# Performance work log

Hardware: AMD Instinct MI355X
Metric: run time of the kernel (lower is better)

Reference implementation:

```python
import jax, jax.numpy as jnp
import numpy as np

T, B, OBS, H, A = 128, 256, 128, 512, 18
LSTM_IN = H + A + 1  # trunk_out + one_hot(a) + r


def setup_inputs() -> dict:
    key = jax.random.key(0)
    ks = jax.random.split(key, 24)

    def rn(k, shape, scale=0.05):
        return jax.random.normal(k, shape, dtype=jnp.float32) * scale

    inp = {
        "o": jax.random.normal(ks[0], (T, B, OBS), dtype=jnp.float32),
        "a": jax.random.randint(ks[1], (T, B), 0, A, dtype=jnp.int32),
        "r": jax.random.normal(ks[2], (T, B), dtype=jnp.float32),
        "done": (jax.random.uniform(ks[3], (T, B)) < 0.05).astype(jnp.float32),
        "h0": jax.random.normal(ks[4], (B, H), dtype=jnp.float32) * 0.1,
        "c0": jax.random.normal(ks[5], (B, H), dtype=jnp.float32) * 0.1,
        # trunk
        "tW0": rn(ks[6], (OBS, H)), "tb0": jnp.zeros((H,), jnp.float32),
        "tW1": rn(ks[7], (H, H)), "tb1": jnp.zeros((H,), jnp.float32),
        # LSTM (PyTorch layout: gates stacked as [i, f, g, o])
        "W_ih": rn(ks[8], (4 * H, LSTM_IN)), "W_hh": rn(ks[9], (4 * H, H)),
        "b_ih": jnp.zeros((4 * H,), jnp.float32), "b_hh": jnp.zeros((4 * H,), jnp.float32),
        # advantage head
        "aW0": rn(ks[10], (H, H)), "ab0": jnp.zeros((H,), jnp.float32),
        "aW1": rn(ks[11], (H, A)), "ab1": jnp.zeros((A,), jnp.float32),
        # value head
        "vW0": rn(ks[12], (H, H)), "vb0": jnp.zeros((H,), jnp.float32),
        "vW1": rn(ks[13], (H, 1)), "vb1": jnp.zeros((1,), jnp.float32),
    }
    return inp


def _forward(o, a, r, done, h0, c0, tW0, tb0, tW1, tb1,
             W_ih, W_hh, b_ih, b_hh, aW0, ab0, aW1, ab1, vW0, vb0, vW1, vb1):
    # shared trunk: two Linear+ReLU layers, vectorized over T*B
    hidden = jax.nn.relu(jnp.einsum('tbi,ih->tbh', o, tW0) + tb0)
    hidden = jax.nn.relu(jnp.einsum('tbi,ih->tbh', hidden, tW1) + tb1)
    a_oh = jax.nn.one_hot(a, A, dtype=jnp.float32)          # [T,B,A]
    x = jnp.concatenate([hidden, r[..., None], a_oh], -1)    # [T,B,LSTM_IN]

    # precompute input projection for all steps (not state-dependent)
    xg = jnp.einsum('tbi,gi->tbg', x, W_ih) + b_ih + b_hh    # [T,B,4H]

    def step(carry, inp):
        h, c = carry
        xg_t, d_t = inp
        keep = (1.0 - d_t)[:, None]                          # per-step done reset
        h, c = h * keep, c * keep
        gates = xg_t + h @ W_hh.T                            # [B,4H]
        i, f, g, og = jnp.split(gates, 4, axis=-1)
        c = jax.nn.sigmoid(f) * c + jax.nn.sigmoid(i) * jnp.tanh(g)
        h = jax.nn.sigmoid(og) * jnp.tanh(c)
        return (h, c), h

    (hT, cT), hs = jax.lax.scan(step, (h0, c0), (xg, done))  # hs: [T,B,H]

    ah = jax.nn.relu(jnp.einsum('tbh,hk->tbk', hs, aW0) + ab0)
    adv = jnp.einsum('tbk,ka->tba', ah, aW1) + ab1            # [T,B,A]
    vh = jax.nn.relu(jnp.einsum('tbh,hk->tbk', hs, vW0) + vb0)
    val = jnp.einsum('tbk,kv->tbv', vh, vW1) + vb1            # [T,B,1]
    q = val + (adv - adv.mean(axis=-1, keepdims=True))
    return q, hT, cT


def reference(o, a, r, done, h0, c0, tW0, tb0, tW1, tb1,
              W_ih, W_hh, b_ih, b_hh, aW0, ab0, aW1, ab1, vW0, vb0, vW1, vb1):
    return _forward(o, a, r, done, h0, c0, tW0, tb0, tW1, tb1,
                    W_ih, W_hh, b_ih, b_hh, aW0, ab0, aW1, ab1, vW0, vb0, vW1, vb1)
```

## Files before the change

### kernel.cpp

```cpp
#include <hip/hip_runtime.h>
#include <cstdint>

typedef unsigned short u16;
typedef unsigned int u32;
typedef unsigned long long u64;
typedef float f32x4 __attribute__((ext_vector_type(4)));
typedef short s16x8 __attribute__((ext_vector_type(8)));

#define DEV static __device__ __forceinline__

#define TT 128
#define BB 256
#define OBSD 128
#define HHD 512
#define AD 18
#define GGD 2048
#define MMD 32768

DEV u16 f2bf(float f) {
  u32 u = __builtin_bit_cast(u32, f);
  u += 0x7fffu + ((u >> 16) & 1u);
  return (u16)(u >> 16);
}
DEV float bf2f(u16 h) { return __builtin_bit_cast(float, ((u32)h) << 16); }

DEV f32x4 mfma16x16x32(s16x8 a, s16x8 b, f32x4 c) {
  asm("v_mfma_f32_16x16x32_bf16 %0, %1, %2, %0" : "+v"(c) : "v"(a), "v"(b));
  return c;
}
DEV void fence_mfma_read(f32x4& x) { asm volatile("s_nop 7" : "+v"(x)); }
DEV void fence_mfma_srcc(f32x4& x) { asm volatile("s_nop 1" : "+v"(x)); }
DEV void fence_valu_srca(s16x8& x) { asm volatile("s_nop 1" : "+v"(x)); }

typedef __attribute__((address_space(3))) char lds_char;
typedef __attribute__((address_space(1))) const char gl_char;
DEV void gload16(const char* g, char* l) {
  __builtin_amdgcn_global_load_lds((const gl_char*)g, (lds_char*)l, 16, 0, 0);
}

DEV float sigm(float x) { return 1.f / (1.f + __expf(-x)); }
DEV float tanh_fast(float x) {
  float t = __expf(-2.f * fabsf(x));
  float r = (1.f - t) / (1.f + t);
  return copysignf(r, x);
}

constexpr size_t OFF_FLAGS = 0;
constexpr size_t OFF_HRING = 524288;
constexpr size_t OFF_TW0T  = 1048576;
constexpr size_t OFF_TW1T  = 1179648;
constexpr size_t OFF_AW0T  = 1703936;
constexpr size_t OFF_VW0T  = 2228224;
constexpr size_t OFF_AW1T  = 2752512;
constexpr size_t OFF_VW1T  = 2770944;
constexpr size_t OFF_WIH   = 2772992;
constexpr size_t OFF_WHH   = 4870144;
constexpr size_t OFF_BSUM  = 6967296;
constexpr size_t OFF_WRC   = 6975488;
constexpr size_t OFF_WEMB  = 6983680;
constexpr size_t OFF_BCAT  = 7131136;
constexpr size_t OFF_OBF   = 8388608;
constexpr size_t OFF_BUF1  = 16777216;
constexpr size_t OFF_BUF2  = 50331648;
constexpr size_t OFF_BUF3  = 83886080;

__global__ __launch_bounds__(256) void prep(
    const float* __restrict__ o, const float* __restrict__ tW0,
    const float* __restrict__ tW1, const float* __restrict__ aW0,
    const float* __restrict__ vW0, const float* __restrict__ aW1,
    const float* __restrict__ vW1, const float* __restrict__ Wih,
    const float* __restrict__ WhhF, const float* __restrict__ bih,
    const float* __restrict__ bhh, const float* __restrict__ h0,
    const float* __restrict__ ab0, const float* __restrict__ vb0,
    u16* __restrict__ o_bf, u16* __restrict__ tW0T, u16* __restrict__ tW1T,
    u16* __restrict__ aW0T, u16* __restrict__ vW0T, u16* __restrict__ aW1T,
    u16* __restrict__ vW1T, u16* __restrict__ WihB, u16* __restrict__ WhhB,
    float* __restrict__ bsum, float* __restrict__ wrc, float* __restrict__ wemb,
    float* __restrict__ bcat, u16* __restrict__ hring)
{
  const int total = 4178432;
  for (int id = blockIdx.x * 256 + threadIdx.x; id < total; id += gridDim.x * 256) {
    int i = id;
    if (i < 1048576) {
      float4 v = ((const float4*)o)[i];
      u16* dst = o_bf + (size_t)i * 4;
      dst[0] = f2bf(v.x); dst[1] = f2bf(v.y); dst[2] = f2bf(v.z); dst[3] = f2bf(v.w);
      continue;
    }
    i -= 1048576;
    if (i < 65536)  { int n = i >> 7, k = i & 127; tW0T[i] = f2bf(tW0[k * 512 + n]); continue; }
    i -= 65536;
    if (i < 262144) { int n = i >> 9, k = i & 511; tW1T[i] = f2bf(tW1[k * 512 + n]); continue; }
    i -= 262144;
    if (i < 262144) { int n = i >> 9, k = i & 511; aW0T[i] = f2bf(aW0[k * 512 + n]); continue; }
    i -= 262144;
    if (i < 262144) { int n = i >> 9, k = i & 511; vW0T[i] = f2bf(vW0[k * 512 + n]); continue; }
    i -= 262144;
    if (i < 9216)   { int n = i >> 9, k = i & 511; aW1T[i] = f2bf(aW1[k * 18 + n]); continue; }
    i -= 9216;
    if (i < 512)    { vW1T[i] = f2bf(vW1[i]); continue; }
    i -= 512;
    if (i < 1048576){ int g = i >> 9, k = i & 511; WihB[i] = f2bf(Wih[g * 531 + k]); continue; }
    i -= 1048576;
    if (i < 1048576){ WhhB[i] = f2bf(WhhF[i]); continue; }
    i -= 1048576;
    if (i < 2048)   { bsum[i] = bih[i] + bhh[i]; wrc[i] = Wih[i * 531 + 512]; continue; }
    i -= 2048;
    if (i < 36864)  { int j = i >> 11, g = i & 2047; wemb[i] = Wih[g * 531 + 513 + j]; continue; }
    i -= 36864;
    if (i < 1024)   { bcat[i] = (i < 512) ? ab0[i] : vb0[i - 512]; continue; }
    i -= 1024;
    { hring[i] = f2bf(h0[i]); }
  }
}

template<int MODE>
__global__ __launch_bounds__(256) void gemm_bt(
    const u16* __restrict__ A, const u16* __restrict__ Bt, u16* __restrict__ C,
    int Mdim, int Ndim, int Kdim,
    const float* __restrict__ bias,
    const float* __restrict__ wrc, const float* __restrict__ wemb,
    const float* __restrict__ rin, const int* __restrict__ ain)
{
  __shared__ __align__(16) char smem[32768];
  const int tid = threadIdx.x;
  const int nTn = Ndim >> 7;
  int wg = blockIdx.x;
  {
    const int per = gridDim.x >> 3;
    wg = (wg & 7) * per + (wg >> 3);
  }
  const int tm = wg / nTn, tn = wg % nTn;
  const int wid = tid >> 6, lane = tid & 63;
  const int wr = wid >> 1, wc = wid & 1;
  const int l15 = lane & 15, l4 = lane >> 4;

  f32x4 acc[4][4];
#pragma unroll
  for (int i = 0; i < 4; ++i)
#pragma unroll
    for (int j = 0; j < 4; ++j) acc[i][j] = f32x4{0.f, 0.f, 0.f, 0.f};

  const int srow = lane >> 3;
  const int scolb = ((lane & 7) * 16) ^ (srow << 4);
  const size_t kd2 = (size_t)Kdim * 2;
  const char* Abase = (const char*)(A + (size_t)tm * 128 * Kdim);
  const char* Bbase = (const char*)(Bt + (size_t)tn * 128 * Kdim);
  const char* ga[4]; const char* gb[4]; char* la[4]; char* lb[4];
#pragma unroll
  for (int j = 0; j < 4; ++j) {
    const int row = wid * 32 + j * 8 + srow;
    ga[j] = Abase + (size_t)row * kd2 + scolb;
    gb[j] = Bbase + (size_t)row * kd2 + scolb;
    la[j] = smem + wid * 4096 + j * 1024;
    lb[j] = smem + 16384 + wid * 4096 + j * 1024;
  }

  for (int k0 = 0; k0 < Kdim; k0 += 64) {
    const size_t kb = (size_t)k0 * 2;
#pragma unroll
    for (int j = 0; j < 4; ++j) {
      gload16(ga[j] + kb, la[j]);
      gload16(gb[j] + kb, lb[j]);
    }
    __syncthreads();
#pragma unroll
    for (int kk = 0; kk < 2; ++kk) {
      s16x8 af[4], bfr[4];
#pragma unroll
      for (int i = 0; i < 4; ++i) {
        int ar = wr * 64 + i * 16 + l15;
        af[i] = *(const s16x8*)(smem + ((ar * 128 + kk * 64 + l4 * 16) ^ ((ar & 7) << 4)));
        int br = wc * 64 + i * 16 + l15;
        bfr[i] = *(const s16x8*)(smem + 16384 + ((br * 128 + kk * 64 + l4 * 16) ^ ((br & 7) << 4)));
      }
#pragma unroll
      for (int i = 0; i < 4; ++i)
#pragma unroll
        for (int j = 0; j < 4; ++j)
          acc[i][j] = mfma16x16x32(af[i], bfr[j], acc[i][j]);
    }
    __syncthreads();
  }

#pragma unroll
  for (int i = 0; i < 4; ++i)
#pragma unroll
    for (int j = 0; j < 4; ++j) fence_mfma_read(acc[i][j]);

#pragma unroll
  for (int i = 0; i < 4; ++i) {
    const int rowb = tm * 128 + wr * 64 + i * 16 + l4 * 4;
    float rv[4]; int av[4];
    if (MODE == 1) {
#pragma unroll
      for (int r = 0; r < 4; ++r) { rv[r] = rin[rowb + r]; av[r] = ain[rowb + r]; }
    }
#pragma unroll
    for (int j = 0; j < 4; ++j) {
      const int col = tn * 128 + wc * 64 + j * 16 + l15;
      const float bs = bias[col];
      if (MODE == 0) {
#pragma unroll
        for (int r = 0; r < 4; ++r) {
          float x = acc[i][j][r] + bs;
          x = fmaxf(x, 0.f);
          C[(size_t)(rowb + r) * Ndim + col] = f2bf(x);
        }
      } else {
        const float wcv = wrc[col];
#pragma unroll
        for (int r = 0; r < 4; ++r) {
          float x = acc[i][j][r] + bs + rv[r] * wcv + wemb[av[r] * GGD + col];
          C[(size_t)(rowb + r) * Ndim + col] = f2bf(x);
        }
      }
    }
  }
}

__global__ __launch_bounds__(256, 1) void lstm_seq(
    const u16* __restrict__ xg, const u16* __restrict__ WhhB,
    const u16* __restrict__ WheadT, const float* __restrict__ done,
    const float* __restrict__ c0, const float* __restrict__ bcat,
    u16* __restrict__ hring, u16* __restrict__ ah, u16* __restrict__ vh,
    float* __restrict__ hT, float* __restrict__ cT, u32* __restrict__ cnt)
{
  __shared__ __align__(16) char wsm[65536];
  __shared__ __align__(16) char whd[32768];
  const int tid = threadIdx.x;
  const int bg = blockIdx.x & 3;
  const int ug = blockIdx.x >> 2;
  const int b0 = bg * 64;
  const int u0 = ug * 16;
  const int hc0 = ug * 32;

#pragma unroll
  for (int i = 0; i < 16; ++i) {
    int idx = i * 256 + tid;
    int lr = idx >> 6, c8 = idx & 63;
    int g = lr >> 4, uu = lr & 15;
    uint4 v = *(const uint4*)(WhhB + (size_t)(g * 512 + u0 + uu) * 512 + c8 * 8);
    *(uint4*)(wsm + ((lr * 1024 + c8 * 16) ^ ((lr & 7) << 4))) = v;
  }
#pragma unroll
  for (int i = 0; i < 8; ++i) {
    int idx = i * 256 + tid;
    int lr = idx >> 6, c8 = idx & 63;
    uint4 v = *(const uint4*)(WheadT + (size_t)(hc0 + lr) * 512 + c8 * 8);
    *(uint4*)(whd + ((lr * 1024 + c8 * 16) ^ ((lr & 7) << 4))) = v;
  }
  __syncthreads();

  const int wid = tid >> 6, lane = tid & 63;
  const int l15 = lane & 15, l4 = lane >> 4;
  const int mrow = wid * 16 + l4 * 4;
  const int afrow = b0 + wid * 16 + l15;
  const int u = u0 + l15;
  u32* const mycnt = cnt + ((bg << 2) | wid) * TT;

  u16* const hvout = (ug < 16) ? ah : vh;
  const int hcl = (ug < 16) ? hc0 : hc0 - 512;
  float bcv[2];
#pragma unroll
  for (int j = 0; j < 2; ++j) bcv[j] = bcat[hc0 + j * 16 + l15];

  float creg[4], kc[4];
#pragma unroll
  for (int r = 0; r < 4; ++r) {
    creg[r] = c0[(size_t)(b0 + mrow + r) * HHD + u];
    kc[r] = 1.f - done[b0 + mrow + r];
  }
  u64 am;
  { float dn = done[afrow]; am = (dn != 0.f) ? 0ull : ~0ull; }

  u16 xpf[16];
#pragma unroll
  for (int g = 0; g < 4; ++g)
#pragma unroll
    for (int r = 0; r < 4; ++r)
      xpf[g * 4 + r] = xg[(size_t)(b0 + mrow + r) * GGD + g * HHD + u];

  for (int t = 0; t < TT; ++t) {
    const u16* hsrc = hring + (size_t)(t & 1) * (BB * HHD);
    u16* hdst = hring + (size_t)((t + 1) & 1) * (BB * HHD);

    f32x4 acc[4];
#pragma unroll
    for (int g = 0; g < 4; ++g)
#pragma unroll
      for (int r = 0; r < 4; ++r)
        acc[g][r] = bf2f(xpf[g * 4 + r]);
#pragma unroll
    for (int g = 0; g < 4; ++g) fence_mfma_srcc(acc[g]);

    u64 aflo[16], afhi[16];
    const u64* hb = (const u64*)(hsrc + (size_t)afrow * HHD);
#pragma unroll
    for (int kk = 0; kk < 16; ++kk) {
      aflo[kk] = __hip_atomic_load(hb + kk * 8 + l4 * 2,
                                   __ATOMIC_RELAXED, __HIP_MEMORY_SCOPE_AGENT);
      afhi[kk] = __hip_atomic_load(hb + kk * 8 + l4 * 2 + 1,
                                   __ATOMIC_RELAXED, __HIP_MEMORY_SCOPE_AGENT);
    }
#pragma unroll
    for (int kk = 0; kk < 16; ++kk) {
      union { u64 q[2]; s16x8 v; } tmp;
      tmp.q[0] = aflo[kk] & am; tmp.q[1] = afhi[kk] & am;
      s16x8 a = tmp.v;
      fence_valu_srca(a);
#pragma unroll
      for (int g = 0; g < 4; ++g) {
        int br = g * 16 + l15;
        s16x8 b = *(const s16x8*)(wsm + ((br * 1024 + kk * 64 + l4 * 16) ^ ((br & 7) << 4)));
        acc[g] = mfma16x16x32(a, b, acc[g]);
      }
    }
#pragma unroll
    for (int g = 0; g < 4; ++g) fence_mfma_read(acc[g]);

    float hv_[4], cv_[4];
#pragma unroll
    for (int r = 0; r < 4; ++r) {
      float iv = sigm(acc[0][r]);
      float fv = sigm(acc[1][r]);
      float gv = tanh_fast(acc[2][r]);
      float ov = sigm(acc[3][r]);
      float c = fv * (creg[r] * kc[r]) + iv * gv;
      float h = ov * tanh_fast(c);
      creg[r] = c; cv_[r] = c; hv_[r] = h;
    }

    {
      u32 pw[4];
#pragma unroll
      for (int r = 0; r < 4; ++r) {
        u16 ob = f2bf(hv_[r]);
        u16 pb = (u16)__shfl_xor((int)ob, 1, 64);
        pw[r] = ((l15 & 1) == 0) ? ((u32)ob | ((u32)pb << 16))
                                 : ((u32)pb | ((u32)ob << 16));
      }
      const int rb = (l15 & 1) * 2;
      u32* hd32 = (u32*)hdst;
      const int col2 = (u0 + (l15 & ~1)) >> 1;
      __hip_atomic_store(&hd32[(size_t)(b0 + mrow + rb) * 256 + col2], pw[rb],
                         __ATOMIC_RELAXED, __HIP_MEMORY_SCOPE_AGENT);
      __hip_atomic_store(&hd32[(size_t)(b0 + mrow + rb + 1) * 256 + col2], pw[rb + 1],
                         __ATOMIC_RELAXED, __HIP_MEMORY_SCOPE_AGENT);
    }
    asm volatile("s_waitcnt vmcnt(0)" ::: "memory");
    if (lane == 0)
      __hip_atomic_fetch_add(&mycnt[t], 1u,
                             __ATOMIC_RELAXED, __HIP_MEMORY_SCOPE_AGENT);

    if (t > 0) {
      f32x4 acch[2];
#pragma unroll
      for (int j = 0; j < 2; ++j)
#pragma unroll
        for (int r = 0; r < 4; ++r) acch[j][r] = bcv[j];
#pragma unroll
      for (int j = 0; j < 2; ++j) fence_mfma_srcc(acch[j]);
#pragma unroll
      for (int kk = 0; kk < 16; ++kk) {
        union { u64 q[2]; s16x8 v; } tmp;
        tmp.q[0] = aflo[kk]; tmp.q[1] = afhi[kk];
        s16x8 a = tmp.v;
#pragma unroll
        for (int j = 0; j < 2; ++j) {
          int br = j * 16 + l15;
          s16x8 b = *(const s16x8*)(whd + ((br * 1024 + kk * 64 + l4 * 16) ^ ((br & 7) << 4)));
          acch[j] = mfma16x16x32(a, b, acch[j]);
        }
      }
#pragma unroll
      for (int j = 0; j < 2; ++j) fence_mfma_read(acch[j]);
#pragma unroll
      for (int j = 0; j < 2; ++j)
#pragma unroll
        for (int r = 0; r < 4; ++r) {
          float x = fmaxf(acch[j][r], 0.f);
          hvout[((size_t)(t - 1) * BB + b0 + mrow + r) * 512 + hcl + j * 16 + l15] = f2bf(x);
        }
    }
    if (t == TT - 1) {
#pragma unroll
      for (int r = 0; r < 4; ++r) {
        hT[(size_t)(b0 + mrow + r) * HHD + u] = hv_[r];
        cT[(size_t)(b0 + mrow + r) * HHD + u] = cv_[r];
      }
    } else {
#pragma unroll
      for (int g = 0; g < 4; ++g)
#pragma unroll
        for (int r = 0; r < 4; ++r)
          xpf[g * 4 + r] = xg[((size_t)(t + 1) * BB + b0 + mrow + r) * GGD + g * HHD + u];
#pragma unroll
      for (int r = 0; r < 4; ++r)
        kc[r] = 1.f - done[(size_t)(t + 1) * BB + b0 + mrow + r];
      float dn = done[(size_t)(t + 1) * BB + afrow];
      am = (dn != 0.f) ? 0ull : ~0ull;
    }

    while (__hip_atomic_load(&mycnt[t],
                             __ATOMIC_RELAXED, __HIP_MEMORY_SCOPE_AGENT) < 32u)
      __builtin_amdgcn_s_sleep(1);
  }

  {
    const u16* hfin = hring + (size_t)(TT & 1) * (BB * HHD);
    u64 aflo[16], afhi[16];
    const u64* hb = (const u64*)(hfin + (size_t)afrow * HHD);
#pragma unroll
    for (int kk = 0; kk < 16; ++kk) {
      aflo[kk] = __hip_atomic_load(hb + kk * 8 + l4 * 2,
                                   __ATOMIC_RELAXED, __HIP_MEMORY_SCOPE_AGENT);
      afhi[kk] = __hip_atomic_load(hb + kk * 8 + l4 * 2 + 1,
                                   __ATOMIC_RELAXED, __HIP_MEMORY_SCOPE_AGENT);
    }
    f32x4 acch[2];
#pragma unroll
    for (int j = 0; j < 2; ++j)
#pragma unroll
      for (int r = 0; r < 4; ++r) acch[j][r] = bcv[j];
#pragma unroll
    for (int j = 0; j < 2; ++j) fence_mfma_srcc(acch[j]);
#pragma unroll
    for (int kk = 0; kk < 16; ++kk) {
      union { u64 q[2]; s16x8 v; } tmp;
      tmp.q[0] = aflo[kk]; tmp.q[1] = afhi[kk];
      s16x8 a = tmp.v;
#pragma unroll
      for (int j = 0; j < 2; ++j) {
        int br = j * 16 + l15;
        s16x8 b = *(const s16x8*)(whd + ((br * 1024 + kk * 64 + l4 * 16) ^ ((br & 7) << 4)));
        acch[j] = mfma16x16x32(a, b, acch[j]);
      }
    }
#pragma unroll
    for (int j = 0; j < 2; ++j) fence_mfma_read(acch[j]);
#pragma unroll
    for (int j = 0; j < 2; ++j)
#pragma unroll
      for (int r = 0; r < 4; ++r) {
        float x = fmaxf(acch[j][r], 0.f);
        hvout[((size_t)(TT - 1) * BB + b0 + mrow + r) * 512 + hcl + j * 16 + l15] = f2bf(x);
      }
  }
}

__global__ __launch_bounds__(256) void head_final(
    const u16* __restrict__ ah, const u16* __restrict__ vh,
    const u16* __restrict__ aW1T, const u16* __restrict__ vW1T,
    const float* __restrict__ ab1, const float* __restrict__ vb1,
    float* __restrict__ q)
{
  __shared__ __align__(16) u16 wa[AD * HHD];
  __shared__ __align__(16) u16 wv[HHD];
  const int tid = threadIdx.x;
  for (int i = tid; i < AD * HHD / 8; i += 256) ((uint4*)wa)[i] = ((const uint4*)aW1T)[i];
  for (int i = tid; i < HHD / 8; i += 256) ((uint4*)wv)[i] = ((const uint4*)vW1T)[i];
  __syncthreads();
  const int wid = tid >> 6, lane = tid & 63;
  for (int row = blockIdx.x * 4 + wid; row < MMD; row += gridDim.x * 4) {
    uint4 va = *(const uint4*)(ah + (size_t)row * 512 + lane * 8);
    uint4 vv = *(const uint4*)(vh + (size_t)row * 512 + lane * 8);
    const u16* pa = (const u16*)&va;
    const u16* pv = (const u16*)&vv;
    float af[8], vf[8];
#pragma unroll
    for (int j = 0; j < 8; ++j) { af[j] = bf2f(pa[j]); vf[j] = bf2f(pv[j]); }
    float accs[19];
#pragma unroll
    for (int n = 0; n < 19; ++n) accs[n] = 0.f;
#pragma unroll
    for (int n = 0; n < AD; ++n) {
      const u16* w = wa + n * HHD + lane * 8;
#pragma unroll
      for (int j = 0; j < 8; ++j) accs[n] += af[j] * bf2f(w[j]);
    }
    {
      const u16* w = wv + lane * 8;
#pragma unroll
      for (int j = 0; j < 8; ++j) accs[18] += vf[j] * bf2f(w[j]);
    }
#pragma unroll
    for (int n = 0; n < 19; ++n) {
#pragma unroll
      for (int off = 32; off > 0; off >>= 1)
        accs[n] += __shfl_xor(accs[n], off, 64);
    }
    if (lane == 0) {
      float s = 0.f;
      float advv[AD];
#pragma unroll
      for (int n = 0; n < AD; ++n) { advv[n] = accs[n] + ab1[n]; s += advv[n]; }
      float val = accs[18] + vb1[0];
      float mean = s * (1.f / 18.f);
#pragma unroll
      for (int n = 0; n < AD; ++n) q[(size_t)row * AD + n] = val + advv[n] - mean;
    }
  }
}

extern "C" void kernel_launch(void* const* d_in, const int* in_sizes, int n_in,
                              void* d_out, int out_size, void* d_ws, size_t ws_size,
                              hipStream_t stream) {
  const float* o    = (const float*)d_in[0];
  const int*   a    = (const int*)d_in[1];
  const float* r    = (const float*)d_in[2];
  const float* done = (const float*)d_in[3];
  const float* h0   = (const float*)d_in[4];
  const float* c0   = (const float*)d_in[5];
  const float* tW0  = (const float*)d_in[6];
  const float* tb0  = (const float*)d_in[7];
  const float* tW1  = (const float*)d_in[8];
  const float* tb1  = (const float*)d_in[9];
  const float* Wih  = (const float*)d_in[10];
  const float* Whh  = (const float*)d_in[11];
  const float* bih  = (const float*)d_in[12];
  const float* bhh  = (const float*)d_in[13];
  const float* aW0  = (const float*)d_in[14];
  const float* ab0  = (const float*)d_in[15];
  const float* aW1  = (const float*)d_in[16];
  const float* ab1  = (const float*)d_in[17];
  const float* vW0  = (const float*)d_in[18];
  const float* vb0  = (const float*)d_in[19];
  const float* vW1  = (const float*)d_in[20];
  const float* vb1  = (const float*)d_in[21];
  (void)in_sizes; (void)n_in; (void)ws_size;

  char* ws = (char*)d_ws;
  u32* cnt    = (u32*)(ws + OFF_FLAGS);
  u16* hring  = (u16*)(ws + OFF_HRING);
  u16* tW0T   = (u16*)(ws + OFF_TW0T);
  u16* tW1T   = (u16*)(ws + OFF_TW1T);
  u16* aW0T   = (u16*)(ws + OFF_AW0T);
  u16* vW0T   = (u16*)(ws + OFF_VW0T);
  u16* aW1T   = (u16*)(ws + OFF_AW1T);
  u16* vW1T   = (u16*)(ws + OFF_VW1T);
  u16* WihB   = (u16*)(ws + OFF_WIH);
  u16* WhhB   = (u16*)(ws + OFF_WHH);
  float* bsum = (float*)(ws + OFF_BSUM);
  float* wrc  = (float*)(ws + OFF_WRC);
  float* wemb = (float*)(ws + OFF_WEMB);
  float* bcat = (float*)(ws + OFF_BCAT);
  u16* o_bf   = (u16*)(ws + OFF_OBF);
  u16* buf1   = (u16*)(ws + OFF_BUF1);
  u16* buf2   = (u16*)(ws + OFF_BUF2);
  u16* buf3   = (u16*)(ws + OFF_BUF3);

  float* qout = (float*)d_out;
  float* hT   = qout + (size_t)TT * BB * AD;
  float* cT   = hT + (size_t)BB * HHD;

  hipMemsetAsync(cnt, 0, 65536, stream);
  prep<<<2048, 256, 0, stream>>>(o, tW0, tW1, aW0, vW0, aW1, vW1, Wih, Whh,
                                 bih, bhh, h0, ab0, vb0,
                                 o_bf, tW0T, tW1T, aW0T, vW0T, aW1T, vW1T,
                                 WihB, WhhB, bsum, wrc, wemb, bcat, hring);
  gemm_bt<0><<<1024, 256, 0, stream>>>(o_bf, tW0T, buf1, MMD, 512, 128, tb0,
                                       nullptr, nullptr, nullptr, nullptr);
  gemm_bt<0><<<1024, 256, 0, stream>>>(buf1, tW1T, buf2, MMD, 512, 512, tb1,
                                       nullptr, nullptr, nullptr, nullptr);
  gemm_bt<1><<<4096, 256, 0, stream>>>(buf2, WihB, buf3, MMD, 2048, 512, bsum,
                                       wrc, wemb, r, a);
  lstm_seq<<<128, 256, 0, stream>>>(buf3, WhhB, aW0T, done, c0, bcat, hring,
                                    buf1 , buf2 , hT, cT, cnt);
  head_final<<<2048, 256, 0, stream>>>(buf1, buf2, aW1T, vW1T, ab1, vb1, qout);
}
```

Baseline: 1.012 ms.

## Fuse input-projection GEMM into LSTM scan kernel with per-tile ready flags

The separate xg GEMM launch is folded into one kernel with the recurrent scan. Extra blocks compute the projection tiles and store them with agent-scope atomic stores, then bump a per-tile flag. The LSTM blocks spin on those flags before prefetching each step's gate inputs. The goal is to hide the projection GEMM behind the serial recurrence instead of running it beforehand. In exchange it relies on all recurrent blocks being resident alongside the producers, adds flag-polling overhead, and lets producer blocks contend with the scan for bandwidth and CUs.

```diff
diff --git a/kernel.cpp b/kernel.cpp
--- a/kernel.cpp
+++ b/kernel.cpp
@@ -46,6 +46,7 @@
 }
 
 constexpr size_t OFF_FLAGS = 0;
+constexpr size_t OFF_XGFLG = 32768;
 constexpr size_t OFF_HRING = 524288;
 constexpr size_t OFF_TW0T  = 1048576;
 constexpr size_t OFF_TW1T  = 1179648;
@@ -114,13 +115,9 @@
   }
 }
 
-template<int MODE>
 __global__ __launch_bounds__(256) void gemm_bt(
     const u16* __restrict__ A, const u16* __restrict__ Bt, u16* __restrict__ C,
-    int Mdim, int Ndim, int Kdim,
-    const float* __restrict__ bias,
-    const float* __restrict__ wrc, const float* __restrict__ wemb,
-    const float* __restrict__ rin, const int* __restrict__ ain)
+    int Mdim, int Ndim, int Kdim, const float* __restrict__ bias)
 {
   __shared__ __align__(16) char smem[32768];
   const int tid = threadIdx.x;
@@ -191,49 +188,137 @@
 #pragma unroll
   for (int i = 0; i < 4; ++i) {
     const int rowb = tm * 128 + wr * 64 + i * 16 + l4 * 4;
-    float rv[4]; int av[4];
-    if (MODE == 1) {
-#pragma unroll
-      for (int r = 0; r < 4; ++r) { rv[r] = rin[rowb + r]; av[r] = ain[rowb + r]; }
-    }
 #pragma unroll
     for (int j = 0; j < 4; ++j) {
       const int col = tn * 128 + wc * 64 + j * 16 + l15;
       const float bs = bias[col];
-      if (MODE == 0) {
-#pragma unroll
-        for (int r = 0; r < 4; ++r) {
-          float x = acc[i][j][r] + bs;
-          x = fmaxf(x, 0.f);
-          C[(size_t)(rowb + r) * Ndim + col] = f2bf(x);
+#pragma unroll
+      for (int r = 0; r < 4; ++r) {
+        float x = acc[i][j][r] + bs;
+        x = fmaxf(x, 0.f);
+        C[(size_t)(rowb + r) * Ndim + col] = f2bf(x);
+      }
+    }
+  }
+}
+
+__global__ __launch_bounds__(256, 1) void scan_fused(
+    const u16* __restrict__ hid, const u16* __restrict__ WihB,
+    const float* __restrict__ rin, const int* __restrict__ ain,
+    const float* __restrict__ bsum, const float* __restrict__ wrcv,
+    const float* __restrict__ wemb, u16* __restrict__ xg,
+    const u16* __restrict__ WhhB, const u16* __restrict__ WheadT,
+    const float* __restrict__ done, const float* __restrict__ c0,
+    const float* __restrict__ bcat, u16* __restrict__ hring,
+    u16* __restrict__ ah, u16* __restrict__ vh,
+    float* __restrict__ hT, float* __restrict__ cT,
+    u32* __restrict__ cnt, u32* __restrict__ xgflag)
+{
+  __shared__ __align__(16) char lds[98304];
+  const int tid = threadIdx.x;
+  const int wid = tid >> 6, lane = tid & 63;
+  const int l15 = lane & 15, l4 = lane >> 4;
+
+  if (blockIdx.x >= 128) {
+    char* smem = lds;
+    const int wr = wid >> 1, wc = wid & 1;
+    const int srow = lane >> 3;
+    const int scolb = ((lane & 7) * 16) ^ (srow << 4);
+    const int wkr = blockIdx.x - 128;
+    for (int idx = wkr; idx < 4096; idx += 512) {
+      const int tm = idx >> 4, tn = idx & 15;
+      f32x4 acc[4][4];
+#pragma unroll
+      for (int i = 0; i < 4; ++i)
+#pragma unroll
+        for (int j = 0; j < 4; ++j) acc[i][j] = f32x4{0.f, 0.f, 0.f, 0.f};
+      const char* Abase = (const char*)(hid + (size_t)tm * 128 * 512);
+      const char* Bbase = (const char*)(WihB + (size_t)tn * 128 * 512);
+      const char* ga[4]; const char* gb[4]; char* la[4]; char* lb[4];
+#pragma unroll
+      for (int j = 0; j < 4; ++j) {
+        const int row = wid * 32 + j * 8 + srow;
+        ga[j] = Abase + (size_t)row * 1024 + scolb;
+        gb[j] = Bbase + (size_t)row * 1024 + scolb;
+        la[j] = smem + wid * 4096 + j * 1024;
+        lb[j] = smem + 16384 + wid * 4096 + j * 1024;
+      }
+      for (int k0 = 0; k0 < 512; k0 += 64) {
+        const size_t kb = (size_t)k0 * 2;
+#pragma unroll
+        for (int j = 0; j < 4; ++j) {
+          gload16(ga[j] + kb, la[j]);
+          gload16(gb[j] + kb, lb[j]);
         }
-      } else {
-        const float wcv = wrc[col];
-#pragma unroll
-        for (int r = 0; r < 4; ++r) {
-          float x = acc[i][j][r] + bs + rv[r] * wcv + wemb[av[r] * GGD + col];
-          C[(size_t)(rowb + r) * Ndim + col] = f2bf(x);
+        __syncthreads();
+#pragma unroll
+        for (int kk = 0; kk < 2; ++kk) {
+          s16x8 af[4], bfr[4];
+#pragma unroll
+          for (int i = 0; i < 4; ++i) {
+            int ar = wr * 64 + i * 16 + l15;
+            af[i] = *(const s16x8*)(smem + ((ar * 128 + kk * 64 + l4 * 16) ^ ((ar & 7) << 4)));
+            int br = wc * 64 + i * 16 + l15;
+            bfr[i] = *(const s16x8*)(smem + 16384 + ((br * 128 + kk * 64 + l4 * 16) ^ ((br & 7) << 4)));
+          }
+#pragma unroll
+          for (int i = 0; i < 4; ++i)
+#pragma unroll
+            for (int j = 0; j < 4; ++j)
+              acc[i][j] = mfma16x16x32(af[i], bfr[j], acc[i][j]);
         }
-      }
-    }
-  }
-}
-
-__global__ __launch_bounds__(256, 1) void lstm_seq(
-    const u16* __restrict__ xg, const u16* __restrict__ WhhB,
-    const u16* __restrict__ WheadT, const float* __restrict__ done,
-    const float* __restrict__ c0, const float* __restrict__ bcat,
-    u16* __restrict__ hring, u16* __restrict__ ah, u16* __restrict__ vh,
-    float* __restrict__ hT, float* __restrict__ cT, u32* __restrict__ cnt)
-{
-  __shared__ __align__(16) char wsm[65536];
-  __shared__ __align__(16) char whd[32768];
-  const int tid = threadIdx.x;
+        __syncthreads();
+      }
+#pragma unroll
+      for (int i = 0; i < 4; ++i)
+#pragma unroll
+        for (int j = 0; j < 4; ++j) fence_mfma_read(acc[i][j]);
+
+#pragma unroll
+      for (int i = 0; i < 4; ++i) {
+        const int rowb = tm * 128 + wr * 64 + i * 16 + l4 * 4;
+        float rv[4]; int av[4];
+#pragma unroll
+        for (int r = 0; r < 4; ++r) { rv[r] = rin[rowb + r]; av[r] = ain[rowb + r]; }
+#pragma unroll
+        for (int j = 0; j < 4; ++j) {
+          const int col = tn * 128 + wc * 64 + j * 16 + l15;
+          const float bs = bsum[col];
+          const float wcv = wrcv[col];
+          u32 pw[4];
+#pragma unroll
+          for (int r = 0; r < 4; ++r) {
+            float x = acc[i][j][r] + bs + rv[r] * wcv + wemb[av[r] * GGD + col];
+            u16 ob = f2bf(x);
+            u16 pb = (u16)__shfl_xor((int)ob, 1, 64);
+            pw[r] = ((l15 & 1) == 0) ? ((u32)ob | ((u32)pb << 16))
+                                     : ((u32)pb | ((u32)ob << 16));
+          }
+          const int rb = (l15 & 1) * 2;
+          u32* c32 = (u32*)xg;
+          const int col2 = (col & ~1) >> 1;
+          __hip_atomic_store(&c32[(size_t)(rowb + rb) * 1024 + col2], pw[rb],
+                             __ATOMIC_RELAXED, __HIP_MEMORY_SCOPE_AGENT);
+          __hip_atomic_store(&c32[(size_t)(rowb + rb + 1) * 1024 + col2], pw[rb + 1],
+                             __ATOMIC_RELAXED, __HIP_MEMORY_SCOPE_AGENT);
+        }
+      }
+      asm volatile("s_waitcnt vmcnt(0)" ::: "memory");
+      if (lane == 0)
+        __hip_atomic_fetch_add(&xgflag[idx], 1u,
+                               __ATOMIC_RELAXED, __HIP_MEMORY_SCOPE_AGENT);
+    }
+    return;
+  }
+
+  char* wsm = lds;
+  char* whd = lds + 65536;
   const int bg = blockIdx.x & 3;
   const int ug = blockIdx.x >> 2;
   const int b0 = bg * 64;
   const int u0 = ug * 16;
   const int hc0 = ug * 32;
+  const int ugr = ug >> 3;
 
 #pragma unroll
   for (int i = 0; i < 16; ++i) {
@@ -252,8 +337,6 @@
   }
   __syncthreads();
 
-  const int wid = tid >> 6, lane = tid & 63;
-  const int l15 = lane & 15, l4 = lane >> 4;
   const int mrow = wid * 16 + l4 * 4;
   const int afrow = b0 + wid * 16 + l15;
   const int u = u0 + l15;
@@ -274,6 +357,17 @@
   u64 am;
   { float dn = done[afrow]; am = (dn != 0.f) ? 0ull : ~0ull; }
 
+  {
+    const int tm0 = bg >> 1;
+    for (;;) {
+      u32 v = 4;
+      if (lane < 4)
+        v = __hip_atomic_load(&xgflag[tm0 * 16 + lane * 4 + ugr],
+                              __ATOMIC_RELAXED, __HIP_MEMORY_SCOPE_AGENT);
+      if (__all(v >= 4)) break;
+      __builtin_amdgcn_s_sleep(4);
+    }
+  }
   u16 xpf[16];
 #pragma unroll
   for (int g = 0; g < 4; ++g)
@@ -390,6 +484,17 @@
         cT[(size_t)(b0 + mrow + r) * HHD + u] = cv_[r];
       }
     } else {
+      {
+        const int tm1 = 2 * (t + 1) + (bg >> 1);
+        for (;;) {
+          u32 v = 4;
+          if (lane < 4)
+            v = __hip_atomic_load(&xgflag[tm1 * 16 + lane * 4 + ugr],
+                                  __ATOMIC_RELAXED, __HIP_MEMORY_SCOPE_AGENT);
+          if (__all(v >= 4)) break;
+          __builtin_amdgcn_s_sleep(2);
+        }
+      }
 #pragma unroll
       for (int g = 0; g < 4; ++g)
 #pragma unroll
@@ -532,6 +637,7 @@
 
   char* ws = (char*)d_ws;
   u32* cnt    = (u32*)(ws + OFF_FLAGS);
+  u32* xgflag = (u32*)(ws + OFF_XGFLG);
   u16* hring  = (u16*)(ws + OFF_HRING);
   u16* tW0T   = (u16*)(ws + OFF_TW0T);
   u16* tW1T   = (u16*)(ws + OFF_TW1T);
@@ -559,13 +665,11 @@
                                  bih, bhh, h0, ab0, vb0,
                                  o_bf, tW0T, tW1T, aW0T, vW0T, aW1T, vW1T,
                                  WihB, WhhB, bsum, wrc, wemb, bcat, hring);
-  gemm_bt<0><<<1024, 256, 0, stream>>>(o_bf, tW0T, buf1, MMD, 512, 128, tb0,
-                                       nullptr, nullptr, nullptr, nullptr);
-  gemm_bt<0><<<1024, 256, 0, stream>>>(buf1, tW1T, buf2, MMD, 512, 512, tb1,
-                                       nullptr, nullptr, nullptr, nullptr);
-  gemm_bt<1><<<4096, 256, 0, stream>>>(buf2, WihB, buf3, MMD, 2048, 512, bsum,
-                                       wrc, wemb, r, a);
-  lstm_seq<<<128, 256, 0, stream>>>(buf3, WhhB, aW0T, done, c0, bcat, hring,
-                                    buf1 , buf2 , hT, cT, cnt);
+  gemm_bt<<<1024, 256, 0, stream>>>(o_bf, tW0T, buf1, MMD, 512, 128, tb0);
+  gemm_bt<<<1024, 256, 0, stream>>>(buf1, tW1T, buf2, MMD, 512, 512, tb1);
+  scan_fused<<<640, 256, 0, stream>>>(buf2 , WihB, r, a, bsum, wrc, wemb,
+                                      buf3 , WhhB, aW0T, done, c0, bcat,
+                                      hring, buf1 , buf2 , hT, cT,
+                                      cnt, xgflag);
   head_final<<<2048, 256, 0, stream>>>(buf1, buf2, aW1T, vW1T, ab1, vb1, qout);
 }
```

Result: slower. 1.425 ms (+40.9%).
